# Optimization experiments

Measured on AMD Instinct MI355X. Metric: run time of the kernel, lower is better.

## Reference

```python
import jax, jax.numpy as jnp
import numpy as np

N_NODES = 50000
N_EDGES = 800000
D_IN = 512
D_HID = 64
D_OUT = 40


def setup_inputs() -> dict:
    key = jax.random.key(0)
    ks = jax.random.split(key, 8)
    x = jax.random.normal(ks[0], (N_NODES, D_IN), dtype=jnp.float32)
    edge_index = jax.random.randint(ks[1], (2, N_EDGES), 0, N_NODES, dtype=jnp.int32)
    w_mul = jax.random.uniform(ks[2], (N_EDGES,), dtype=jnp.float32)
    s1 = 1.0 / np.sqrt(D_IN)
    s2 = 1.0 / np.sqrt(D_HID)
    W1 = jax.random.uniform(ks[3], (D_IN, D_HID), minval=-s1, maxval=s1, dtype=jnp.float32)
    b1 = jax.random.uniform(ks[4], (D_HID,), minval=-s1, maxval=s1, dtype=jnp.float32)
    W2 = jax.random.uniform(ks[5], (D_HID, D_OUT), minval=-s2, maxval=s2, dtype=jnp.float32)
    b2 = jax.random.uniform(ks[6], (D_OUT,), minval=-s2, maxval=s2, dtype=jnp.float32)
    return {"x": x, "edge_index": edge_index, "w_mul": w_mul,
            "W1": W1, "b1": b1, "W2": W2, "b2": b2}


def _conv(h, src, dst, w_mul, W, b, n_nodes):
    # linear transform, then gather-scale-scatter-add (PyG aggr='add')
    h = h @ W + b                      # [N, d_out]
    msg = w_mul[:, None] * h[src]      # [E, d_out] gather + scale
    return jax.ops.segment_sum(msg, dst, num_segments=n_nodes)  # scatter-add


def reference(x, edge_index, w_mul, W1, b1, W2, b2):
    n_nodes = x.shape[0]
    src, dst = edge_index[0], edge_index[1]  # flow: source_to_target
    h = _conv(x, src, dst, w_mul, W1, b1, n_nodes)
    h = jax.nn.relu(h)
    h = _conv(h, src, dst, w_mul, W2, b2, n_nodes)
    return jax.nn.log_softmax(h, axis=1)
```

## Files before the change

kernel.cpp:

```cpp
#include <hip/hip_runtime.h>
#include <math.h>

#define D_IN  512
#define D_HID 64
#define D_OUT 40
#define CAP   64

typedef __attribute__((ext_vector_type(8))) short bf16x8;
typedef __attribute__((ext_vector_type(4))) float f32x4;

static __device__ __forceinline__ unsigned short f2bf(float f) {
    unsigned u = __float_as_uint(f);
    return (unsigned short)((u + 0x7FFF + ((u >> 16) & 1)) >> 16);
}
static __device__ __forceinline__ float bf2f(unsigned short h) {
    return __uint_as_float(((unsigned)h) << 16);
}

__global__ __launch_bounds__(256)
void prep_all(int* __restrict__ cursor, const float* __restrict__ W1,
              unsigned short* __restrict__ w1T, const float* __restrict__ W2,
              unsigned short* __restrict__ w2T, int N) {
    const int i = blockIdx.x * blockDim.x + threadIdx.x;
    if (i < N) cursor[i] = 0;
    const int j = i - N;
    if (j >= 0 && j < D_IN * D_HID) {
        const int k = j >> 6, col = j & 63;
        w1T[col * D_IN + k] = f2bf(W1[j]);
    }
    const int l = j - D_IN * D_HID;
    if (l >= 0 && l < 48 * D_HID) {
        const int col = l >> 6, k = l & 63;
        w2T[l] = (col < D_OUT) ? f2bf(W2[k * D_OUT + col]) : 0;
    }
}

__global__ __launch_bounds__(256)
void fat1(const float* __restrict__ x, const unsigned short* __restrict__ w1T,
          const float* __restrict__ b1, unsigned short* __restrict__ h1,
          const int* __restrict__ src, const int* __restrict__ dstA,
          const float* __restrict__ wm, int* __restrict__ cursor,
          unsigned* __restrict__ edges, int E, int N, int sBlocks) {
    __shared__ unsigned char lds[16384];
    const int t = threadIdx.x;

    if ((int)blockIdx.x < sBlocks) {
        const int slice = (N + 7) >> 3;
        const int lo = (blockIdx.x & 7) * slice;
        const int hi = min(N, lo + slice);
        const int nChunk = sBlocks >> 3;
        const int per = (E + nChunk - 1) / nChunk;
        const int beg = ((int)blockIdx.x >> 3) * per;
        const int end = min(E, beg + per);
        for (int e = beg + t; e < end; e += 256) {
            const int d = dstA[e];
            if (d >= lo && d < hi) {
                const int pos = atomicAdd(&cursor[d], 1);
                if (pos < CAP)
                    edges[(size_t)d * CAP + pos] =
                        ((unsigned)src[e] << 16) | (unsigned)f2bf(wm[e]);
            }
        }
        return;
    }

    const int lane = t & 63;
    const int wv = t >> 6;
    const int nodeBase = ((int)blockIdx.x - sBlocks) * 64;

    const int row0 = t >> 3, slot0 = t & 7;
    const int row1 = (t + 256) >> 3, slot1 = (t + 256) & 7;
    int gn0 = nodeBase + row0; if (gn0 >= N) gn0 = N - 1;
    int gn1 = nodeBase + row1; if (gn1 >= N) gn1 = N - 1;
    const float* xp0 = x + (size_t)gn0 * D_IN + slot0 * 8;
    const float* xp1 = x + (size_t)gn1 * D_IN + slot1 * 8;
    const unsigned short* wp0 = w1T + (size_t)row0 * D_IN + slot0 * 8;
    const unsigned short* wp1 = w1T + (size_t)row1 * D_IN + slot1 * 8;

    f32x4 acc[4];
#pragma unroll
    for (int cg = 0; cg < 4; ++cg) acc[cg] = (f32x4){0.f, 0.f, 0.f, 0.f};

    for (int k0 = 0; k0 < D_IN; k0 += 64) {
        const float4 xa0 = *reinterpret_cast<const float4*>(xp0 + k0);
        const float4 xb0 = *reinterpret_cast<const float4*>(xp0 + k0 + 4);
        const float4 xa1 = *reinterpret_cast<const float4*>(xp1 + k0);
        const float4 xb1 = *reinterpret_cast<const float4*>(xp1 + k0 + 4);
        const uint4  wr0 = *reinterpret_cast<const uint4*>(wp0 + k0);
        const uint4  wr1 = *reinterpret_cast<const uint4*>(wp1 + k0);

        uint4 p;
        p.x = (unsigned)f2bf(xa0.x) | ((unsigned)f2bf(xa0.y) << 16);
        p.y = (unsigned)f2bf(xa0.z) | ((unsigned)f2bf(xa0.w) << 16);
        p.z = (unsigned)f2bf(xb0.x) | ((unsigned)f2bf(xb0.y) << 16);
        p.w = (unsigned)f2bf(xb0.z) | ((unsigned)f2bf(xb0.w) << 16);
        *reinterpret_cast<uint4*>(lds + row0 * 128 + ((slot0 << 4) ^ ((row0 & 7) << 4))) = p;
        p.x = (unsigned)f2bf(xa1.x) | ((unsigned)f2bf(xa1.y) << 16);
        p.y = (unsigned)f2bf(xa1.z) | ((unsigned)f2bf(xa1.w) << 16);
        p.z = (unsigned)f2bf(xb1.x) | ((unsigned)f2bf(xb1.y) << 16);
        p.w = (unsigned)f2bf(xb1.z) | ((unsigned)f2bf(xb1.w) << 16);
        *reinterpret_cast<uint4*>(lds + row1 * 128 + ((slot1 << 4) ^ ((row1 & 7) << 4))) = p;
        *reinterpret_cast<uint4*>(lds + 8192 + row0 * 128 + ((slot0 << 4) ^ ((row0 & 7) << 4))) = wr0;
        *reinterpret_cast<uint4*>(lds + 8192 + row1 * 128 + ((slot1 << 4) ^ ((row1 & 7) << 4))) = wr1;
        __syncthreads();

        const int fr = lane & 15;
        const int fc = lane >> 4;
#pragma unroll
        for (int s = 0; s < 2; ++s) {
            const int slot = s * 4 + fc;
            const int arow = wv * 16 + fr;
            const bf16x8 afrag = *reinterpret_cast<const bf16x8*>(
                lds + arow * 128 + ((slot << 4) ^ ((arow & 7) << 4)));
#pragma unroll
            for (int cg = 0; cg < 4; ++cg) {
                const int brow = cg * 16 + fr;
                const bf16x8 bfrag = *reinterpret_cast<const bf16x8*>(
                    lds + 8192 + brow * 128 + ((slot << 4) ^ ((brow & 7) << 4)));
                acc[cg] = __builtin_amdgcn_mfma_f32_16x16x32_bf16(afrag, bfrag, acc[cg], 0, 0, 0);
            }
        }
        __syncthreads();
    }

    const int fr = lane & 15;
    const int rq = lane >> 4;
#pragma unroll
    for (int cg = 0; cg < 4; ++cg) {
        const int col = cg * 16 + fr;
        const float bb = b1[col];
#pragma unroll
        for (int r = 0; r < 4; ++r) {
            const int node = nodeBase + wv * 16 + rq * 4 + r;
            if (node < N)
                h1[(size_t)node * D_HID + col] = f2bf(acc[cg][r] + bb);
        }
    }
}

__global__ __launch_bounds__(256)
void agg_hid(const unsigned short* __restrict__ h, const unsigned* __restrict__ edges,
             const int* __restrict__ count, unsigned short* __restrict__ agg1, int N) {
    const int lane = threadIdx.x & 63;
    const int wv   = (threadIdx.x >> 6);
    const int slice = (N + 7) >> 3;
    const int local = ((int)blockIdx.x >> 3) * 4 + wv;
    if (local >= slice) return;
    const int n = ((int)blockIdx.x & 7) * slice + local;
    if (n >= N) return;
    const unsigned er = edges[(size_t)n * CAP + lane];
    const int cnt = min(count[n], CAP);
    float acc = 0.f;
    int j = 0;
    for (; j + 8 <= cnt; j += 8) {
        unsigned p[8];
#pragma unroll
        for (int u = 0; u < 8; ++u) p[u] = (unsigned)__shfl((int)er, j + u);
        float v[8];
#pragma unroll
        for (int u = 0; u < 8; ++u) v[u] = bf2f(h[(size_t)(p[u] >> 16) * D_HID + lane]);
#pragma unroll
        for (int u = 0; u < 8; ++u)
            acc += bf2f((unsigned short)(p[u] & 0xffff)) * v[u];
    }
    for (; j < cnt; ++j) {
        const unsigned p0 = (unsigned)__shfl((int)er, j);
        acc += bf2f((unsigned short)(p0 & 0xffff)) *
               bf2f(h[(size_t)(p0 >> 16) * D_HID + lane]);
    }
    agg1[(size_t)n * D_HID + lane] = f2bf(fmaxf(acc, 0.f));
}

__global__ __launch_bounds__(256)
void gemm2_mfma(const unsigned short* __restrict__ agg1,
                const unsigned short* __restrict__ w2T,
                const float* __restrict__ b2, unsigned short* __restrict__ h2, int N) {
    __shared__ unsigned char lds[8192 + 6144];
    const int t = threadIdx.x;
    const int lane = t & 63;
    const int wv = t >> 6;
    const int nodeBase = blockIdx.x * 64;

#pragma unroll
    for (int hh = 0; hh < 2; ++hh) {
        const int g = t + hh * 256;
        const int row = g >> 3, slot = g & 7;
        int gn = nodeBase + row; if (gn >= N) gn = N - 1;
        const uint4 p = *reinterpret_cast<const uint4*>(agg1 + (size_t)gn * D_HID + slot * 8);
        *reinterpret_cast<uint4*>(lds + row * 128 + ((slot << 4) ^ ((row & 7) << 4))) = p;
    }
    for (int g = t; g < 384; g += 256) {
        const int row = g >> 3, slot = g & 7;
        const uint4 p = *reinterpret_cast<const uint4*>(w2T + (size_t)row * D_HID + slot * 8);
        *reinterpret_cast<uint4*>(lds + 8192 + row * 128 + ((slot << 4) ^ ((row & 7) << 4))) = p;
    }
    __syncthreads();

    f32x4 acc[3];
#pragma unroll
    for (int cg = 0; cg < 3; ++cg) acc[cg] = (f32x4){0.f, 0.f, 0.f, 0.f};

    const int fr = lane & 15;
    const int fc = lane >> 4;
#pragma unroll
    for (int s = 0; s < 2; ++s) {
        const int slot = s * 4 + fc;
        const int arow = wv * 16 + fr;
        const bf16x8 afrag = *reinterpret_cast<const bf16x8*>(
            lds + arow * 128 + ((slot << 4) ^ ((arow & 7) << 4)));
#pragma unroll
        for (int cg = 0; cg < 3; ++cg) {
            const int brow = cg * 16 + fr;
            const bf16x8 bfrag = *reinterpret_cast<const bf16x8*>(
                lds + 8192 + brow * 128 + ((slot << 4) ^ ((brow & 7) << 4)));
            acc[cg] = __builtin_amdgcn_mfma_f32_16x16x32_bf16(afrag, bfrag, acc[cg], 0, 0, 0);
        }
    }

    const int rq = lane >> 4;
#pragma unroll
    for (int cg = 0; cg < 3; ++cg) {
        const int col = cg * 16 + fr;
        if (col < D_OUT) {
            const float bb = b2[col];
#pragma unroll
            for (int r = 0; r < 4; ++r) {
                const int node = nodeBase + wv * 16 + rq * 4 + r;
                if (node < N)
                    h2[(size_t)node * D_OUT + col] = f2bf(acc[cg][r] + bb);
            }
        }
    }
}

__global__ __launch_bounds__(256)
void agg40_lsm(const unsigned short* __restrict__ h2, const unsigned* __restrict__ edges,
               const int* __restrict__ count, float* __restrict__ out, int N) {
    const int lane = threadIdx.x & 63;
    const int col  = (lane < D_OUT) ? lane : 0;
    const int wv   = (threadIdx.x >> 6);
    const int slice = (N + 7) >> 3;
    const int local = ((int)blockIdx.x >> 3) * 4 + wv;
    if (local >= slice) return;
    const int n = ((int)blockIdx.x & 7) * slice + local;
    if (n >= N) return;
    const unsigned er = edges[(size_t)n * CAP + lane];
    const int cnt = min(count[n], CAP);
    float acc = 0.f;
    int j = 0;
    for (; j + 8 <= cnt; j += 8) {
        unsigned p[8];
#pragma unroll
        for (int u = 0; u < 8; ++u) p[u] = (unsigned)__shfl((int)er, j + u);
        float v[8];
#pragma unroll
        for (int u = 0; u < 8; ++u) v[u] = bf2f(h2[(size_t)(p[u] >> 16) * D_OUT + col]);
#pragma unroll
        for (int u = 0; u < 8; ++u)
            acc += bf2f((unsigned short)(p[u] & 0xffff)) * v[u];
    }
    for (; j < cnt; ++j) {
        const unsigned p0 = (unsigned)__shfl((int)er, j);
        acc += bf2f((unsigned short)(p0 & 0xffff)) *
               bf2f(h2[(size_t)(p0 >> 16) * D_OUT + col]);
    }
    const float v = (lane < D_OUT) ? acc : -INFINITY;
    float m = v;
#pragma unroll
    for (int o = 32; o > 0; o >>= 1) m = fmaxf(m, __shfl_xor(m, o, 64));
    float s = (lane < D_OUT) ? __expf(v - m) : 0.f;
#pragma unroll
    for (int o = 32; o > 0; o >>= 1) s += __shfl_xor(s, o, 64);
    if (lane < D_OUT) out[(size_t)n * D_OUT + lane] = v - m - __logf(s);
}

extern "C" void kernel_launch(void* const* d_in, const int* in_sizes, int n_in,
                              void* d_out, int out_size, void* d_ws, size_t ws_size,
                              hipStream_t stream) {
    const float* x   = (const float*)d_in[0];
    const int*   ei  = (const int*)d_in[1];
    const float* wm  = (const float*)d_in[2];
    const float* W1  = (const float*)d_in[3];
    const float* b1  = (const float*)d_in[4];
    const float* W2  = (const float*)d_in[5];
    const float* b2  = (const float*)d_in[6];

    const int N = in_sizes[0] / D_IN;
    const int E = in_sizes[2];
    const int* srcIdx = ei;
    const int* dstIdx = ei + E;

    unsigned short* w1T    = (unsigned short*)d_ws;
    unsigned short* h1bf   = w1T + (size_t)D_HID * D_IN;
    unsigned short* agg1bf = h1bf + (size_t)N * D_HID;
    unsigned* edges        = (unsigned*)(agg1bf + (size_t)N * D_HID);
    int*   cursor          = (int*)(edges + (size_t)N * CAP);
    unsigned short* w2T    = (unsigned short*)(cursor + N);
    unsigned short* h2bf   = h1bf;
    float* out             = (float*)d_out;

    const int g1Blocks = (N + 63) / 64;
    const int sBlocks  = 1024;
    const int prepWork = N + D_IN * D_HID + 48 * D_HID;
    const int slice = (N + 7) >> 3;
    const int aggBlocks = ((slice + 3) / 4) * 8;

    prep_all<<<(prepWork + 255) / 256, 256, 0, stream>>>(cursor, W1, w1T, W2, w2T, N);
    fat1<<<sBlocks + g1Blocks, 256, 0, stream>>>(
        x, w1T, b1, h1bf, srcIdx, dstIdx, wm, cursor, edges, E, N, sBlocks);
    agg_hid<<<aggBlocks, 256, 0, stream>>>(h1bf, edges, cursor, agg1bf, N);
    gemm2_mfma<<<g1Blocks, 256, 0, stream>>>(agg1bf, w2T, b2, h2bf, N);
    agg40_lsm<<<aggBlocks, 256, 0, stream>>>(h2bf, edges, cursor, out, N);
}
```

Measured before the change: 118.6 us.

## Split first GEMM over K into two halves with separate combine kernel

The first-layer GEMM blocks now each handle half of the 512-wide reduction, doubling the block count. They write fp32 partial sums to two workspace buffers. A new combine kernel adds the partials plus bias and converts to bf16. This raises parallelism in the x-streaming GEMM but adds extra global memory traffic for the partials and one more kernel launch.

```diff
diff --git a/kernel.cpp b/kernel.cpp
--- a/kernel.cpp
+++ b/kernel.cpp
@@ -37,7 +37,7 @@
 
 __global__ __launch_bounds__(256)
 void fat1(const float* __restrict__ x, const unsigned short* __restrict__ w1T,
-          const float* __restrict__ b1, unsigned short* __restrict__ h1,
+          float* __restrict__ hp0, float* __restrict__ hp1,
           const int* __restrict__ src, const int* __restrict__ dstA,
           const float* __restrict__ wm, int* __restrict__ cursor,
           unsigned* __restrict__ edges, int E, int N, int sBlocks) {
@@ -64,24 +64,29 @@
         return;
     }
 
+    const int gb = (int)blockIdx.x - sBlocks;
+    const int half = gb & 1;
+    const int nodeBase = (gb >> 1) * 64;
+    const int kbase = half * 256;
+    float* __restrict__ hp = half ? hp1 : hp0;
+
     const int lane = t & 63;
     const int wv = t >> 6;
-    const int nodeBase = ((int)blockIdx.x - sBlocks) * 64;
 
     const int row0 = t >> 3, slot0 = t & 7;
     const int row1 = (t + 256) >> 3, slot1 = (t + 256) & 7;
     int gn0 = nodeBase + row0; if (gn0 >= N) gn0 = N - 1;
     int gn1 = nodeBase + row1; if (gn1 >= N) gn1 = N - 1;
-    const float* xp0 = x + (size_t)gn0 * D_IN + slot0 * 8;
-    const float* xp1 = x + (size_t)gn1 * D_IN + slot1 * 8;
-    const unsigned short* wp0 = w1T + (size_t)row0 * D_IN + slot0 * 8;
-    const unsigned short* wp1 = w1T + (size_t)row1 * D_IN + slot1 * 8;
+    const float* xp0 = x + (size_t)gn0 * D_IN + kbase + slot0 * 8;
+    const float* xp1 = x + (size_t)gn1 * D_IN + kbase + slot1 * 8;
+    const unsigned short* wp0 = w1T + (size_t)row0 * D_IN + kbase + slot0 * 8;
+    const unsigned short* wp1 = w1T + (size_t)row1 * D_IN + kbase + slot1 * 8;
 
     f32x4 acc[4];
 #pragma unroll
     for (int cg = 0; cg < 4; ++cg) acc[cg] = (f32x4){0.f, 0.f, 0.f, 0.f};
 
-    for (int k0 = 0; k0 < D_IN; k0 += 64) {
+    for (int k0 = 0; k0 < 256; k0 += 64) {
         const float4 xa0 = *reinterpret_cast<const float4*>(xp0 + k0);
         const float4 xb0 = *reinterpret_cast<const float4*>(xp0 + k0 + 4);
         const float4 xa1 = *reinterpret_cast<const float4*>(xp1 + k0);
@@ -128,14 +133,29 @@
 #pragma unroll
     for (int cg = 0; cg < 4; ++cg) {
         const int col = cg * 16 + fr;
-        const float bb = b1[col];
 #pragma unroll
         for (int r = 0; r < 4; ++r) {
             const int node = nodeBase + wv * 16 + rq * 4 + r;
             if (node < N)
-                h1[(size_t)node * D_HID + col] = f2bf(acc[cg][r] + bb);
-        }
-    }
+                hp[(size_t)node * D_HID + col] = acc[cg][r];
+        }
+    }
+}
+
+__global__ __launch_bounds__(256)
+void combine_k(const float* __restrict__ hp0, const float* __restrict__ hp1,
+               const float* __restrict__ b1, unsigned short* __restrict__ h1, int N) {
+    const int i = blockIdx.x * blockDim.x + threadIdx.x;
+    if (i >= N * 16) return;
+    const float4 a = reinterpret_cast<const float4*>(hp0)[i];
+    const float4 b = reinterpret_cast<const float4*>(hp1)[i];
+    const float4 bb = reinterpret_cast<const float4*>(b1)[i & 15];
+    ushort4 o;
+    o.x = f2bf(a.x + b.x + bb.x);
+    o.y = f2bf(a.y + b.y + bb.y);
+    o.z = f2bf(a.z + b.z + bb.z);
+    o.w = f2bf(a.w + b.w + bb.w);
+    reinterpret_cast<ushort4*>(h1)[i] = o;
 }
 
 __global__ __launch_bounds__(256)
@@ -294,7 +314,9 @@
     unsigned short* h1bf   = w1T + (size_t)D_HID * D_IN;
     unsigned short* agg1bf = h1bf + (size_t)N * D_HID;
     unsigned* edges        = (unsigned*)(agg1bf + (size_t)N * D_HID);
-    int*   cursor          = (int*)(edges + (size_t)N * CAP);
+    float* hp0             = (float*)(edges + (size_t)N * CAP);
+    float* hp1             = hp0 + (size_t)N * D_HID;
+    int*   cursor          = (int*)(hp1 + (size_t)N * D_HID);
     unsigned short* w2T    = (unsigned short*)(cursor + N);
     unsigned short* h2bf   = h1bf;
     float* out             = (float*)d_out;
@@ -306,8 +328,9 @@
     const int aggBlocks = ((slice + 3) / 4) * 8;
 
     prep_all<<<(prepWork + 255) / 256, 256, 0, stream>>>(cursor, W1, w1T, W2, w2T, N);
-    fat1<<<sBlocks + g1Blocks, 256, 0, stream>>>(
-        x, w1T, b1, h1bf, srcIdx, dstIdx, wm, cursor, edges, E, N, sBlocks);
+    fat1<<<sBlocks + 2 * g1Blocks, 256, 0, stream>>>(
+        x, w1T, hp0, hp1, srcIdx, dstIdx, wm, cursor, edges, E, N, sBlocks);
+    combine_k<<<(N * 16 + 255) / 256, 256, 0, stream>>>(hp0, hp1, b1, h1bf, N);
     agg_hid<<<aggBlocks, 256, 0, stream>>>(h1bf, edges, cursor, agg1bf, N);
     gemm2_mfma<<<g1Blocks, 256, 0, stream>>>(agg1bf, w2T, b2, h2bf, N);
     agg40_lsm<<<aggBlocks, 256, 0, stream>>>(h2bf, edges, cursor, out, N);
```

Result: slower. 121.6 us (+2.5%).

## Split first GEMM along K into four partial blocks with a combine kernel

Applied to the files above, without the earlier changes.

The first-layer GEMM is now split along the 512-wide K dimension into four 128-wide chunks, so the launch has four times as many blocks. Each block writes a bf16 partial result to a new workspace region, and a new combine kernel sums the four partials and adds the bias. The aim is more parallelism and better latency hiding for the x-streaming GEMM. In exchange it adds an extra kernel launch, roughly 25 MB of extra partial-result traffic, and extra bf16 rounding of the partial sums.

```diff
diff --git a/kernel.cpp b/kernel.cpp
--- a/kernel.cpp
+++ b/kernel.cpp
@@ -37,7 +37,7 @@
 
 __global__ __launch_bounds__(256)
 void fat1(const float* __restrict__ x, const unsigned short* __restrict__ w1T,
-          const float* __restrict__ b1, unsigned short* __restrict__ h1,
+          unsigned short* __restrict__ hp,
           const int* __restrict__ src, const int* __restrict__ dstA,
           const float* __restrict__ wm, int* __restrict__ cursor,
           unsigned* __restrict__ edges, int E, int N, int sBlocks) {
@@ -64,24 +64,29 @@
         return;
     }
 
+    const int gb = (int)blockIdx.x - sBlocks;
+    const int q = gb & 3;
+    const int nodeBase = (gb >> 2) * 64;
+    const int kbase = q * 128;
+    unsigned short* __restrict__ hq = hp + (size_t)q * N * D_HID;
+
     const int lane = t & 63;
     const int wv = t >> 6;
-    const int nodeBase = ((int)blockIdx.x - sBlocks) * 64;
 
     const int row0 = t >> 3, slot0 = t & 7;
     const int row1 = (t + 256) >> 3, slot1 = (t + 256) & 7;
     int gn0 = nodeBase + row0; if (gn0 >= N) gn0 = N - 1;
     int gn1 = nodeBase + row1; if (gn1 >= N) gn1 = N - 1;
-    const float* xp0 = x + (size_t)gn0 * D_IN + slot0 * 8;
-    const float* xp1 = x + (size_t)gn1 * D_IN + slot1 * 8;
-    const unsigned short* wp0 = w1T + (size_t)row0 * D_IN + slot0 * 8;
-    const unsigned short* wp1 = w1T + (size_t)row1 * D_IN + slot1 * 8;
+    const float* xp0 = x + (size_t)gn0 * D_IN + kbase + slot0 * 8;
+    const float* xp1 = x + (size_t)gn1 * D_IN + kbase + slot1 * 8;
+    const unsigned short* wp0 = w1T + (size_t)row0 * D_IN + kbase + slot0 * 8;
+    const unsigned short* wp1 = w1T + (size_t)row1 * D_IN + kbase + slot1 * 8;
 
     f32x4 acc[4];
 #pragma unroll
     for (int cg = 0; cg < 4; ++cg) acc[cg] = (f32x4){0.f, 0.f, 0.f, 0.f};
 
-    for (int k0 = 0; k0 < D_IN; k0 += 64) {
+    for (int k0 = 0; k0 < 128; k0 += 64) {
         const float4 xa0 = *reinterpret_cast<const float4*>(xp0 + k0);
         const float4 xb0 = *reinterpret_cast<const float4*>(xp0 + k0 + 4);
         const float4 xa1 = *reinterpret_cast<const float4*>(xp1 + k0);
@@ -128,14 +133,49 @@
 #pragma unroll
     for (int cg = 0; cg < 4; ++cg) {
         const int col = cg * 16 + fr;
-        const float bb = b1[col];
 #pragma unroll
         for (int r = 0; r < 4; ++r) {
             const int node = nodeBase + wv * 16 + rq * 4 + r;
             if (node < N)
-                h1[(size_t)node * D_HID + col] = f2bf(acc[cg][r] + bb);
-        }
-    }
+                hq[(size_t)node * D_HID + col] = f2bf(acc[cg][r]);
+        }
+    }
+}
+
+__global__ __launch_bounds__(256)
+void combine_k(const unsigned short* __restrict__ hp, const float* __restrict__ b1,
+               unsigned short* __restrict__ h1, int N) {
+    const int i = blockIdx.x * blockDim.x + threadIdx.x;
+    if (i >= N * 8) return;
+    const size_t stride = (size_t)N * D_HID / 8;
+    const uint4 p0 = reinterpret_cast<const uint4*>(hp)[i];
+    const uint4 p1 = reinterpret_cast<const uint4*>(hp)[i + stride];
+    const uint4 p2 = reinterpret_cast<const uint4*>(hp)[i + 2 * stride];
+    const uint4 p3 = reinterpret_cast<const uint4*>(hp)[i + 3 * stride];
+    const int ch = (i & 7) * 8;
+    const float4 bb0 = *reinterpret_cast<const float4*>(b1 + ch);
+    const float4 bb1 = *reinterpret_cast<const float4*>(b1 + ch + 4);
+    const unsigned w0[4] = {p0.x, p0.y, p0.z, p0.w};
+    const unsigned w1[4] = {p1.x, p1.y, p1.z, p1.w};
+    const unsigned w2[4] = {p2.x, p2.y, p2.z, p2.w};
+    const unsigned w3[4] = {p3.x, p3.y, p3.z, p3.w};
+    const float bia[8] = {bb0.x, bb0.y, bb0.z, bb0.w, bb1.x, bb1.y, bb1.z, bb1.w};
+    uint4 o;
+    unsigned ow[4];
+#pragma unroll
+    for (int d = 0; d < 4; ++d) {
+        const float lo = bf2f((unsigned short)(w0[d] & 0xffff)) +
+                         bf2f((unsigned short)(w1[d] & 0xffff)) +
+                         bf2f((unsigned short)(w2[d] & 0xffff)) +
+                         bf2f((unsigned short)(w3[d] & 0xffff)) + bia[d * 2];
+        const float hi = bf2f((unsigned short)(w0[d] >> 16)) +
+                         bf2f((unsigned short)(w1[d] >> 16)) +
+                         bf2f((unsigned short)(w2[d] >> 16)) +
+                         bf2f((unsigned short)(w3[d] >> 16)) + bia[d * 2 + 1];
+        ow[d] = (unsigned)f2bf(lo) | ((unsigned)f2bf(hi) << 16);
+    }
+    o.x = ow[0]; o.y = ow[1]; o.z = ow[2]; o.w = ow[3];
+    reinterpret_cast<uint4*>(h1)[i] = o;
 }
 
 __global__ __launch_bounds__(256)
@@ -294,7 +334,8 @@
     unsigned short* h1bf   = w1T + (size_t)D_HID * D_IN;
     unsigned short* agg1bf = h1bf + (size_t)N * D_HID;
     unsigned* edges        = (unsigned*)(agg1bf + (size_t)N * D_HID);
-    int*   cursor          = (int*)(edges + (size_t)N * CAP);
+    unsigned short* hp     = (unsigned short*)(edges + (size_t)N * CAP);
+    int*   cursor          = (int*)(hp + (size_t)4 * N * D_HID);
     unsigned short* w2T    = (unsigned short*)(cursor + N);
     unsigned short* h2bf   = h1bf;
     float* out             = (float*)d_out;
@@ -306,8 +347,9 @@
     const int aggBlocks = ((slice + 3) / 4) * 8;
 
     prep_all<<<(prepWork + 255) / 256, 256, 0, stream>>>(cursor, W1, w1T, W2, w2T, N);
-    fat1<<<sBlocks + g1Blocks, 256, 0, stream>>>(
-        x, w1T, b1, h1bf, srcIdx, dstIdx, wm, cursor, edges, E, N, sBlocks);
+    fat1<<<sBlocks + 4 * g1Blocks, 256, 0, stream>>>(
+        x, w1T, hp, srcIdx, dstIdx, wm, cursor, edges, E, N, sBlocks);
+    combine_k<<<(N * 8 + 255) / 256, 256, 0, stream>>>(hp, b1, h1bf, N);
     agg_hid<<<aggBlocks, 256, 0, stream>>>(h1bf, edges, cursor, agg1bf, N);
     gemm2_mfma<<<g1Blocks, 256, 0, stream>>>(agg1bf, w2T, b2, h2bf, N);
     agg40_lsm<<<aggBlocks, 256, 0, stream>>>(h2bf, edges, cursor, out, N);
```

New measurement: 123.7 us. 4.3% more time.
